# Optimization experiments

Measured on AMD Instinct MI355X. Metric: run time of the kernel, lower is better.

The kernel has to match this reference:

```python
import jax, jax.numpy as jnp
import numpy as np

B, T, C, H, HD = 2, 2048, 2048, 16, 128
RD = HD // 2          # rope_dim = 64 (32 complex pairs)
KVR, QR = 512, 1024   # kv_lora_rank, q_lora_rank


def setup_inputs() -> dict:
    key = jax.random.key(0)
    ks = jax.random.split(key, 10)
    s = 0.02
    x = jax.random.normal(ks[0], (B, T, C), jnp.float32)
    w_dq  = jax.random.normal(ks[1], (C, QR),     jnp.float32) * s
    w_uq  = jax.random.normal(ks[2], (QR, H * HD), jnp.float32) * s
    w_dkv = jax.random.normal(ks[3], (C, KVR),    jnp.float32) * s
    w_uk  = jax.random.normal(ks[4], (KVR, H * HD), jnp.float32) * s
    w_uv  = jax.random.normal(ks[5], (KVR, H * HD), jnp.float32) * s
    w_qr  = jax.random.normal(ks[6], (QR, H * RD), jnp.float32) * s
    w_kr  = jax.random.normal(ks[7], (C, H * RD), jnp.float32) * s
    w_o   = jax.random.normal(ks[8], (H * HD, C), jnp.float32) * s
    # rotary frequencies for the rope_dim part (rope_dim//2 = 32 complex freqs)
    inv_freq = 1.0 / (10000.0 ** (jnp.arange(0, RD, 2, dtype=jnp.float32) / RD))
    ang = jnp.arange(T, dtype=jnp.float32)[:, None] * inv_freq[None, :]  # (T, 32)
    return {"x": x, "w_dq": w_dq, "w_uq": w_uq, "w_dkv": w_dkv, "w_uk": w_uk,
            "w_uv": w_uv, "w_qr": w_qr, "w_kr": w_kr, "w_o": w_o,
            "freqs_cos": jnp.cos(ang), "freqs_sin": jnp.sin(ang)}


def _apply_rope(t, cos, sin):
    # t: (B, T, H, rd); cos/sin: (T, rd//2). Complex rotation on adjacent pairs.
    tr, ti = t[..., 0::2], t[..., 1::2]
    c = cos[None, :, None, :]
    s = sin[None, :, None, :]
    out_r = tr * c - ti * s
    out_i = tr * s + ti * c
    return jnp.stack([out_r, out_i], axis=-1).reshape(t.shape)


def reference(x, w_dq, w_uq, w_dkv, w_uk, w_uv, w_qr, w_kr, w_o, freqs_cos, freqs_sin):
    b, t, _ = x.shape
    # low-rank KV path
    c_kv = x @ w_dkv                                   # (B,T,KVR)
    k_c = (c_kv @ w_uk).reshape(b, t, H, HD)
    v   = (c_kv @ w_uv).reshape(b, t, H, HD)
    # low-rank Q path
    c_q = x @ w_dq                                     # (B,T,QR)
    q_c = (c_q @ w_uq).reshape(b, t, H, HD)
    # decoupled rope parts
    q_r = (c_q @ w_qr).reshape(b, t, H, RD)
    k_r = (x @ w_kr).reshape(b, t, H, RD)
    q_r = _apply_rope(q_r, freqs_cos, freqs_sin)
    k_r = _apply_rope(k_r, freqs_cos, freqs_sin)
    # concat content + rope -> head dim D = HD + RD
    q = jnp.concatenate([q_c, q_r], axis=-1).transpose(0, 2, 1, 3)  # (B,H,T,D)
    k = jnp.concatenate([k_c, k_r], axis=-1).transpose(0, 2, 1, 3)
    v = v.transpose(0, 2, 1, 3)                                     # (B,H,T,HD)
    d = q.shape[-1]
    scores = jnp.einsum('bhqd,bhkd->bhqk', q, k) / jnp.sqrt(jnp.float32(d))
    causal = jnp.tril(jnp.ones((t, t), dtype=bool))
    scores = jnp.where(causal[None, None], scores, jnp.float32(-1e30))
    att = jax.nn.softmax(scores, axis=-1)
    out = jnp.einsum('bhqk,bhkd->bhqd', att, v)        # (B,H,T,HD)
    out = out.transpose(0, 2, 1, 3).reshape(b, t, H * HD)
    return out @ w_o
```

## Files before the change

### kernel.cpp

```cpp
#include <hip/hip_runtime.h>

typedef unsigned short ushort_t;
typedef __attribute__((ext_vector_type(8))) short bs8;
typedef __attribute__((ext_vector_type(4))) float f32x4;
typedef __attribute__((ext_vector_type(4))) unsigned short u16x4;

#define DEV __device__ __forceinline__

DEV unsigned short f2bf(float f){
  unsigned u = __float_as_uint(f);
  u += 0x7fffu + ((u >> 16) & 1u);
  return (unsigned short)(u >> 16);
}
DEV float bf2f(unsigned short h){ return __uint_as_float(((unsigned)h) << 16); }

DEV unsigned cvt_pk_bf16(float lo, float hi){
  unsigned r;
  asm volatile("v_cvt_pk_bf16_f32 %0, %1, %2" : "=v"(r) : "v"(lo), "v"(hi));
  return r;
}

DEV void gl2lds16(const void* g, void* l){
  __builtin_amdgcn_global_load_lds((const __attribute__((address_space(1))) void*)g,
                                   (__attribute__((address_space(3))) void*)l, 16, 0, 0);
}

DEV void st_out(ushort_t* C, size_t i, float v){ C[i] = f2bf(v); }
DEV void st_out(float*    C, size_t i, float v){ C[i] = v; }

__global__ __launch_bounds__(256) void cast_x(const float* __restrict__ in,
                                              ushort_t* __restrict__ outb){
  size_t i = ((size_t)blockIdx.x * 256 + threadIdx.x) * 4;
  float4 v = *(const float4*)(in + i);
  u16x4 o;
  o[0] = f2bf(v.x); o[1] = f2bf(v.y); o[2] = f2bf(v.z); o[3] = f2bf(v.w);
  *(u16x4*)(outb + i) = o;
}

__global__ __launch_bounds__(256) void tcast_all(
    const float* __restrict__ s0, const float* __restrict__ s1,
    const float* __restrict__ s2, const float* __restrict__ s3,
    const float* __restrict__ s4, const float* __restrict__ s5,
    const float* __restrict__ s6, const float* __restrict__ s7,
    ushort_t* __restrict__ d0, ushort_t* __restrict__ d1,
    ushort_t* __restrict__ d2, ushort_t* __restrict__ d3,
    ushort_t* __restrict__ d4, ushort_t* __restrict__ d5,
    ushort_t* __restrict__ d6, ushort_t* __restrict__ d7){
  __shared__ float tile[32][33];
  const int bid = blockIdx.x;
  const float* src; ushort_t* dst; int K, N, loc;
  if      (bid <  2048){ src=s0; dst=d0; K=2048; N=1024; loc=bid; }
  else if (bid <  3072){ src=s1; dst=d1; K=2048; N=512;  loc=bid-2048; }
  else if (bid <  5120){ src=s2; dst=d2; K=2048; N=1024; loc=bid-3072; }
  else if (bid <  7168){ src=s3; dst=d3; K=1024; N=2048; loc=bid-5120; }
  else if (bid <  8192){ src=s4; dst=d4; K=1024; N=1024; loc=bid-7168; }
  else if (bid <  9216){ src=s5; dst=d5; K=512;  N=2048; loc=bid-8192; }
  else if (bid < 10240){ src=s6; dst=d6; K=512;  N=2048; loc=bid-9216; }
  else                 { src=s7; dst=d7; K=2048; N=2048; loc=bid-10240; }
  const int nx = N >> 5;
  const int n0 = (loc % nx) << 5, k0 = (loc / nx) << 5;
  const int tx = threadIdx.x & 31, ty = threadIdx.x >> 5;
  for (int r = ty; r < 32; r += 8)
    tile[r][tx] = src[(size_t)(k0 + r) * N + n0 + tx];
  __syncthreads();
  for (int r = ty; r < 32; r += 8)
    dst[(size_t)(n0 + r) * K + k0 + tx] = f2bf(tile[tx][r]);
}

__global__ __launch_bounds__(256) void transpose_v(const ushort_t* __restrict__ v, int ldv,
                                                   ushort_t* __restrict__ vT){
  __shared__ ushort_t tile[32][33];
  int bh = blockIdx.z; int b = bh >> 4, h = bh & 15;
  int t0 = blockIdx.x * 32, d0 = blockIdx.y * 32;
  int tx = threadIdx.x, ty = threadIdx.y;
  for (int r = ty; r < 32; r += 8)
    tile[r][tx] = v[((size_t)(b * 2048 + t0 + r)) * ldv + h * 128 + d0 + tx];
  __syncthreads();
  for (int r = ty; r < 32; r += 8)
    vT[((size_t)bh * 128 + d0 + r) * 2048 + t0 + tx] = tile[tx][r];
}

DEV void gemm_core(const ushort_t* __restrict__ A, int lda,
                   const ushort_t* __restrict__ BT, int K,
                   int m0, int n0, ushort_t* lds, f32x4 (&acc)[8][4]){
  const int tid = threadIdx.x, lane = tid & 63, wid = tid >> 6;
  const int l15 = lane & 15, lhi = lane >> 4;
  const int wr = wid >> 2, wc = wid & 3;

  const int trow = tid >> 3;
  const int tcsrc = (tid & 7) ^ (trow & 7);
  const ushort_t* gA[2][2];
  const ushort_t* gB[2][2];
#pragma unroll
  for (int h = 0; h < 2; ++h)
#pragma unroll
    for (int i = 0; i < 2; ++i){
      gA[h][i] = A  + (size_t)(m0 + h * 128 + i * 64 + trow) * lda + tcsrc * 8;
      gB[h][i] = BT + (size_t)(n0 + h * 128 + i * 64 + trow) * K   + tcsrc * 8;
    }

  auto STAGE_A = [&](int buf, int h, int kt){
    gl2lds16(gA[h][0] + (size_t)kt * 64, lds + buf * 32768 + h * 8192 + tid * 8);
    gl2lds16(gA[h][1] + (size_t)kt * 64, lds + buf * 32768 + h * 8192 + 4096 + tid * 8);
  };
  auto STAGE_B = [&](int buf, int h, int kt){
    gl2lds16(gB[h][0] + (size_t)kt * 64, lds + buf * 32768 + 16384 + h * 8192 + tid * 8);
    gl2lds16(gB[h][1] + (size_t)kt * 64, lds + buf * 32768 + 16384 + h * 8192 + 4096 + tid * 8);
  };

  const int ck0 = ((lhi) ^ (l15 & 7)) << 3;
  const int ck1 = ((4 + lhi) ^ (l15 & 7)) << 3;

  bs8 aF[4][2], bLo[2][2], bHi[2][2];

  auto RDA = [&](int buf, int mq){
#pragma unroll
    for (int m = 0; m < 4; ++m){
      const ushort_t* r = lds + buf * 32768 + wr * 8192 + ((mq + m) * 16 + l15) * 64;
      aF[m][0] = *(const bs8*)(r + ck0);
      aF[m][1] = *(const bs8*)(r + ck1);
    }
  };
  auto RDB = [&](int buf, int nq, bs8 (&br)[2][2]){
#pragma unroll
    for (int n = 0; n < 2; ++n){
      const ushort_t* r = lds + buf * 32768 + 16384 + (wc >> 1) * 8192 +
                          ((wc & 1) * 64 + (nq + n) * 16 + l15) * 64;
      br[n][0] = *(const bs8*)(r + ck0);
      br[n][1] = *(const bs8*)(r + ck1);
    }
  };
  auto MMA = [&](int mq, int nq, bs8 (&br)[2][2]){
    __builtin_amdgcn_s_setprio(1);
#pragma unroll
    for (int m = 0; m < 4; ++m)
#pragma unroll
      for (int n = 0; n < 2; ++n){
        acc[mq + m][nq + n] = __builtin_amdgcn_mfma_f32_16x16x32_bf16(aF[m][0], br[n][0], acc[mq + m][nq + n], 0, 0, 0);
        acc[mq + m][nq + n] = __builtin_amdgcn_mfma_f32_16x16x32_bf16(aF[m][1], br[n][1], acc[mq + m][nq + n], 0, 0, 0);
      }
    __builtin_amdgcn_s_setprio(0);
  };

#define BAR() __builtin_amdgcn_s_barrier()
#define LGK() asm volatile("s_waitcnt lgkmcnt(0)" ::: "memory")
#define VMC4() asm volatile("s_waitcnt vmcnt(4)" ::: "memory")

  const int nkt = K >> 6;
  const int nIter = K >> 7;

  STAGE_A(0, 0, 0); STAGE_A(0, 1, 0); STAGE_B(0, 0, 0); STAGE_B(0, 1, 0);
  STAGE_B(1, 0, 1); STAGE_B(1, 1, 1);
  VMC4();
  BAR();

  for (int it = 0; it < nIter; ++it){
    const int kt1 = 2 * it + 1;
    int kt2 = 2 * it + 2; if (kt2 > nkt - 1) kt2 = nkt - 1;
    int kt3 = 2 * it + 3; if (kt3 > nkt - 1) kt3 = nkt - 1;
    RDA(0, 0); RDB(0, 0, bLo);
    STAGE_A(1, 0, kt1);
    BAR(); LGK(); MMA(0, 0, bLo); BAR();
    RDB(0, 2, bHi);
    STAGE_A(1, 1, kt1);
    BAR(); LGK(); MMA(0, 2, bHi); BAR();
    RDA(0, 4);
    STAGE_B(0, 0, kt2);
    BAR(); LGK(); MMA(4, 0, bLo); BAR();
    STAGE_B(0, 1, kt2);
    BAR(); LGK(); MMA(4, 2, bHi);
    VMC4(); BAR();
    RDA(1, 0); RDB(1, 0, bLo);
    STAGE_A(0, 0, kt2);
    BAR(); LGK(); MMA(0, 0, bLo); BAR();
    RDB(1, 2, bHi);
    STAGE_A(0, 1, kt2);
    BAR(); LGK(); MMA(0, 2, bHi); BAR();
    RDA(1, 4);
    STAGE_B(1, 0, kt3);
    BAR(); LGK(); MMA(4, 0, bLo); BAR();
    STAGE_B(1, 1, kt3);
    BAR(); LGK(); MMA(4, 2, bHi);
    VMC4(); BAR();
  }
#undef BAR
#undef LGK
#undef VMC4
}

template<int EPI, typename OT>
DEV void gemm_epi(f32x4 (&acc)[8][4], OT* __restrict__ C, int N, int m0, int n0,
                  ushort_t* __restrict__ aux,
                  const float* __restrict__ fcp, const float* __restrict__ fsp){
  const int tid = threadIdx.x, lane = tid & 63, wid = tid >> 6;
  const int l15 = lane & 15, lhi = lane >> 4;
  const int wr = wid >> 2, wc = wid & 3;
  const float SC = (EPI == 2) ? (0.07216878364870323f * 1.4426950408889634f) : 1.0f;
  const int RBASE = (EPI == 1) ? 1536 : 2048;
#pragma unroll
  for (int m = 0; m < 8; ++m){
    const int r = m0 + wr * 128 + m * 16 + lhi * 4;
#pragma unroll
    for (int n = 0; n < 4; ++n){
      const int c = n0 + wc * 64 + n * 16 + l15;
      if (EPI == 0){
#pragma unroll
        for (int j = 0; j < 4; ++j)
          st_out(C, (size_t)(r + j) * N + c, acc[m][n][j]);
      } else if ((EPI == 1 && c < 1536)){
#pragma unroll
        for (int j = 0; j < 4; ++j)
          C[(size_t)(r + j) * 1536 + c] = (OT)f2bf(acc[m][n][j]);
      } else if (EPI == 2 && c < 2048){
        int hh = c >> 7, d = c & 127;
#pragma unroll
        for (int j = 0; j < 4; ++j){
          int rr = r + j, bb = rr >> 11, tt = rr & 2047;
          aux[((size_t)(bb * 16 + hh) * 2048 + tt) * 192 + d] = f2bf(acc[m][n][j] * SC);
        }
      } else if (EPI == 3 && c < 2048){
        int hh = c >> 7, d = c & 127;
#pragma unroll
        for (int j = 0; j < 4; ++j){
          int rr = r + j, bb = rr >> 11, tt = rr & 2047;
          aux[((size_t)(bb * 16 + hh) * 2048 + tt) * 192 + d] = f2bf(acc[m][n][j]);
        }
      } else if (EPI == 3){
#pragma unroll
        for (int j = 0; j < 4; ++j)
          C[(size_t)(r + j) * 2048 + (c - 2048)] = (OT)f2bf(acc[m][n][j]);
      } else {
        int cr = c - RBASE;
        int hh = cr >> 6, dr = cr & 63, ii = dr >> 1;
#pragma unroll
        for (int j = 0; j < 4; ++j){
          int rr = r + j, bb = rr >> 11, tt = rr & 2047;
          float v = acc[m][n][j] * SC;
          float pv = __shfl_xor(v, 1);
          float co = fcp[tt * 32 + ii], si = fsp[tt * 32 + ii];
          float o = (l15 & 1) ? fmaf(pv, si, v * co) : fmaf(-pv, si, v * co);
          aux[((size_t)(bb * 16 + hh) * 2048 + tt) * 192 + 128 + dr] = f2bf(o);
        }
      }
    }
  }
}

template<int EPI, typename OT>
__global__ __launch_bounds__(512, 2) void gemm256(const ushort_t* __restrict__ A, int lda,
                                                  const ushort_t* __restrict__ BT,
                                                  OT* __restrict__ C,
                                                  int M, int N, int K,
                                                  ushort_t* __restrict__ aux,
                                                  const float* __restrict__ fcp,
                                                  const float* __restrict__ fsp){
  __shared__ __align__(16) ushort_t lds[65536];
  const int nbx = M >> 8;
  const int nwg = gridDim.x;
  const int orig = blockIdx.x;
  const int wg = (orig & 7) * (nwg >> 3) + (orig >> 3);
  const int m0 = (wg % nbx) << 8;
  const int n0 = (wg / nbx) << 8;
  f32x4 acc[8][4] = {};
  gemm_core(A, lda, BT, K, m0, n0, lds, acc);
  gemm_epi<EPI, OT>(acc, C, N, m0, n0, aux, fcp, fsp);
}

__global__ __launch_bounds__(512, 2) void gemm23(const ushort_t* __restrict__ A2,
                                                 const ushort_t* __restrict__ BT2,
                                                 const ushort_t* __restrict__ A3,
                                                 const ushort_t* __restrict__ BT3,
                                                 ushort_t* __restrict__ vb,
                                                 ushort_t* __restrict__ Qa,
                                                 ushort_t* __restrict__ Ka,
                                                 const float* __restrict__ fcp,
                                                 const float* __restrict__ fsp){
  __shared__ __align__(16) ushort_t lds[65536];
  const int nwg = gridDim.x;
  const int orig = blockIdx.x;
  const int wg = (orig & 7) * (nwg >> 3) + (orig >> 3);
  f32x4 acc[8][4] = {};
  if (wg < 192){
    const int m0 = (wg % 16) << 8, n0 = (wg / 16) << 8;
    gemm_core(A2, 1536, BT2, 1024, m0, n0, lds, acc);
    gemm_epi<2, ushort_t>(acc, nullptr, 3072, m0, n0, Qa, fcp, fsp);
  } else {
    const int g = wg - 192;
    const int m0 = (g % 16) << 8, n0 = (g / 16) << 8;
    gemm_core(A3, 1536, BT3, 512, m0, n0, lds, acc);
    gemm_epi<3, ushort_t>(acc, vb, 4096, m0, n0, Ka, fcp, fsp);
  }
}

__global__ __launch_bounds__(512, 1) void attn_kernel(const ushort_t* __restrict__ Qa,
                                                      const ushort_t* __restrict__ Ka,
                                                      const ushort_t* __restrict__ VT,
                                                      ushort_t* __restrict__ O){
  __shared__ __align__(16) ushort_t lds[40960 + 34816];
  float* fm = (float*)(lds + 40960);
  const int tid = threadIdx.x, lane = tid & 63, wid = tid >> 6;
  const int sw = wid & 3, par = wid >> 2;
  const int bh = blockIdx.x, p = blockIdx.y;
  const int b = bh >> 4, h = bh & 15;
  const int qb0 = 15 - p, qb1 = p;
  const int nkt0 = 2 * qb0 + 2;
  const int NT = 34;
  const int l15 = lane & 15, lhi = lane >> 4;

  const ushort_t* Kbh = Ka + (size_t)bh * 2048 * 192;
  const ushort_t* Vbh = VT + (size_t)bh * 128 * 2048;

  const ushort_t* ksrc[3];
#pragma unroll
  for (int i = 0; i < 3; ++i){
    int c = i * 512 + tid;
    int row = c / 24, col = c % 24;
    int hk = (row & 3) | (((row >> 3) & 1) << 2);
    ksrc[i] = Kbh + (size_t)row * 192 + (col ^ hk) * 8;
  }
  const ushort_t* vsrc[2];
#pragma unroll
  for (int i = 0; i < 2; ++i){
    int c = i * 512 + tid;
    int d = c >> 3, col = c & 7;
    vsrc[i] = Vbh + (size_t)d * 2048 + (col ^ (d & 7)) * 8;
  }

  auto STAGE = [&](int ft, int buf){
    int kt = (ft < nkt0) ? ft : ft - nkt0;
#pragma unroll
    for (int i = 0; i < 3; ++i)
      gl2lds16(ksrc[i] + (size_t)kt * 12288, lds + buf * 12288 + (i * 512 + tid) * 8);
#pragma unroll
    for (int i = 0; i < 2; ++i)
      gl2lds16(vsrc[i] + kt * 64, lds + 24576 + buf * 8192 + (i * 512 + tid) * 8);
  };

  bs8 qf[2][6];
  auto LOADQ = [&](int qb){
#pragma unroll
    for (int qg = 0; qg < 2; ++qg){
      const size_t qrow = ((size_t)bh * 2048 + qb * 128 + sw * 32 + qg * 16 + l15) * 192;
#pragma unroll
      for (int kc = 0; kc < 6; ++kc)
        qf[qg][kc] = *(const bs8*)(Qa + qrow + kc * 32 + lhi * 8);
    }
  };

  f32x4 acc[2][8] = {};
  float mrow[2] = {-1e30f, -1e30f};
  float lrow[2] = {0.f, 0.f};

  auto MERGE_EPI = [&](int qb){
    if (par == 1){
#pragma unroll
      for (int qg = 0; qg < 2; ++qg)
#pragma unroll
        for (int f = 0; f < 8; ++f)
          *(f32x4*)(fm + sw * 4096 + (qg * 8 + f) * 256 + lane * 4) = acc[qg][f];
      f32x4 ml;
      ml[0] = mrow[0]; ml[1] = lrow[0]; ml[2] = mrow[1]; ml[3] = lrow[1];
      *(f32x4*)(fm + 16384 + sw * 256 + lane * 4) = ml;
    }
    __syncthreads();
    if (par == 0){
      f32x4 ml = *(const f32x4*)(fm + 16384 + sw * 256 + lane * 4);
#pragma unroll
      for (int qg = 0; qg < 2; ++qg){
        float m1 = ml[2 * qg], l1 = ml[2 * qg + 1];
        float mm = fmaxf(mrow[qg], m1);
        float f0 = exp2f(mrow[qg] - mm), f1v = exp2f(m1 - mm);
        float rl = 1.0f / (lrow[qg] * f0 + l1 * f1v);
        int t = qb * 128 + sw * 32 + qg * 16 + l15;
#pragma unroll
        for (int f = 0; f < 8; ++f){
          f32x4 a1 = *(const f32x4*)(fm + sw * 4096 + (qg * 8 + f) * 256 + lane * 4);
          u16x4 o;
#pragma unroll
          for (int j = 0; j < 4; ++j)
            o[j] = f2bf((acc[qg][f][j] * f0 + a1[j] * f1v) * rl);
          *(u16x4*)(O + ((size_t)b * 2048 + t) * 2048 + h * 128 + f * 16 + lhi * 4) = o;
        }
      }
    }
  };

  const int hkr = (l15 & 3) | (((l15 >> 2) & 1) << 2);

#define BARR() __builtin_amdgcn_s_barrier()
#define LGK0() asm volatile("s_waitcnt lgkmcnt(0)" ::: "memory")
#define VMC(n) asm volatile("s_waitcnt vmcnt(" #n ")" ::: "memory")

  LOADQ(qb0);
  STAGE(0, 0);
  STAGE(1, 1);
  VMC(5);
  BARR();

  for (int ft = 0; ft < NT; ++ft){
    if (ft == nkt0){
      MERGE_EPI(qb0);
#pragma unroll
      for (int qg = 0; qg < 2; ++qg)
#pragma unroll
        for (int f = 0; f < 8; ++f) acc[qg][f] = (f32x4){0.f, 0.f, 0.f, 0.f};
      mrow[0] = mrow[1] = -1e30f; lrow[0] = lrow[1] = 0.f;
      LOADQ(qb1);
    }
    const int seg = (ft >= nkt0) ? 1 : 0;
    const int kt = seg ? ft - nkt0 : ft;
    const int qb = seg ? qb1 : qb0;
    const int qm0 = qb << 7;
    const int mylast = 2 * qb + (sw >> 1);
    const int cur = ft & 1;
    const ushort_t* Kb = lds + cur * 12288;
    const ushort_t* Vb = lds + 24576 + cur * 8192;

    if (((kt & 1) == par) && kt <= mylast){
      f32x4 s[2][4] = {};
      __builtin_amdgcn_s_setprio(1);
#pragma unroll
      for (int kc = 0; kc < 6; ++kc){
        bs8 kf4[4];
#pragma unroll
        for (int m = 0; m < 4; ++m){
          int row = ((m >> 1) << 5) + ((l15 >> 2) << 3) + ((m & 1) << 2) + (l15 & 3);
          kf4[m] = *(const bs8*)(Kb + row * 192 + (((kc * 4 + lhi) ^ hkr) << 3));
        }
#pragma unroll
        for (int qg = 0; qg < 2; ++qg)
#pragma unroll
          for (int m = 0; m < 4; ++m)
            s[qg][m] = __builtin_amdgcn_mfma_f32_16x16x32_bf16(kf4[m], qf[qg][kc], s[qg][m], 0, 0, 0);
      }
      __builtin_amdgcn_s_setprio(0);

      const bool noMask = (kt * 64 + 63) <= (qm0 + sw * 32);
      bs8 pb[2][2];
#pragma unroll
      for (int qg = 0; qg < 2; ++qg){
        const int qi = qm0 + sw * 32 + qg * 16 + l15;
        float rmax = -3e38f;
#pragma unroll
        for (int m = 0; m < 4; ++m)
#pragma unroll
          for (int j = 0; j < 4; ++j){
            float sv = s[qg][m][j];
            if (!noMask){
              int ki = kt * 64 + ((m >> 1) << 5) + (lhi << 3) + ((m & 1) << 2) + j;
              if (ki > qi) sv = -3e38f;
            }
            s[qg][m][j] = sv;
            rmax = fmaxf(rmax, sv);
          }
        rmax = fmaxf(rmax, __shfl_xor(rmax, 16));
        rmax = fmaxf(rmax, __shfl_xor(rmax, 32));
        if (!__all(rmax <= mrow[qg] + 8.f)){
          float mnew = fmaxf(mrow[qg], rmax);
          float osc = exp2f(mrow[qg] - mnew);
          lrow[qg] *= osc;
#pragma unroll
          for (int f = 0; f < 8; ++f) acc[qg][f] *= osc;
          mrow[qg] = mnew;
        }
        float rsum = 0.f;
#pragma unroll
        for (int m = 0; m < 4; ++m)
#pragma unroll
          for (int j = 0; j < 4; ++j){
            float pv = exp2f(s[qg][m][j] - mrow[qg]);
            s[qg][m][j] = pv;
            rsum += pv;
          }
        rsum += __shfl_xor(rsum, 16);
        rsum += __shfl_xor(rsum, 32);
        lrow[qg] += rsum;

#pragma unroll
        for (int kc2 = 0; kc2 < 2; ++kc2){
          union { bs8 v; unsigned u[4]; } pu;
#pragma unroll
          for (int half = 0; half < 2; ++half){
            const f32x4& sv = s[qg][2 * kc2 + half];
            pu.u[2 * half]     = cvt_pk_bf16(sv[0], sv[1]);
            pu.u[2 * half + 1] = cvt_pk_bf16(sv[2], sv[3]);
          }
          pb[qg][kc2] = pu.v;
        }
      }

      __builtin_amdgcn_s_setprio(1);
#pragma unroll
      for (int kc2 = 0; kc2 < 2; ++kc2)
#pragma unroll
        for (int f = 0; f < 8; ++f){
          bs8 vf = *(const bs8*)(Vb + (f * 16 + l15) * 64 + (((kc2 * 4 + lhi) ^ (l15 & 7)) << 3));
#pragma unroll
          for (int qg = 0; qg < 2; ++qg)
            acc[qg][f] = __builtin_amdgcn_mfma_f32_16x16x32_bf16(vf, pb[qg][kc2], acc[qg][f], 0, 0, 0);
        }
      __builtin_amdgcn_s_setprio(0);
    }

    LGK0();
    BARR();
    if (ft + 2 < NT){
      STAGE(ft + 2, cur);
      VMC(5);
    } else {
      VMC(0);
    }
    BARR();
  }
#undef BARR
#undef LGK0
#undef VMC

  MERGE_EPI(qb1);
}

extern "C" void kernel_launch(void* const* d_in, const int* in_sizes, int n_in,
                              void* d_out, int out_size, void* d_ws, size_t ws_size,
                              hipStream_t stream){
  constexpr int Bc = 2, Tc = 2048, Cc = 2048, Hc = 16, HDc = 128, RDc = 64, KVRc = 512, QRc = 1024;
  constexpr int Mx = Bc * Tc;
  const float* x     = (const float*)d_in[0];
  const float* w_dq  = (const float*)d_in[1];
  const float* w_uq  = (const float*)d_in[2];
  const float* w_dkv = (const float*)d_in[3];
  const float* w_uk  = (const float*)d_in[4];
  const float* w_uv  = (const float*)d_in[5];
  const float* w_qr  = (const float*)d_in[6];
  const float* w_kr  = (const float*)d_in[7];
  const float* w_o   = (const float*)d_in[8];
  const float* fc    = (const float*)d_in[9];
  const float* fs    = (const float*)d_in[10];
  float* out = (float*)d_out;

  char* ws = (char*)d_ws;
  size_t off = 0;
  auto alloc = [&](size_t elems) -> ushort_t* {
    ushort_t* p = (ushort_t*)(ws + off);
    off += ((elems * 2) + 255) & ~(size_t)255;
    return p;
  };
  ushort_t* xb    = alloc((size_t)Mx * Cc);
  ushort_t* wdqT  = alloc((size_t)QRc * Cc);
  ushort_t* wdkvT = alloc((size_t)KVRc * Cc);
  ushort_t* wkrT  = alloc((size_t)(Hc * RDc) * Cc);
  ushort_t* wuqT  = alloc((size_t)(Hc * HDc) * QRc);
  ushort_t* wqrT  = alloc((size_t)(Hc * RDc) * QRc);
  ushort_t* wukT  = alloc((size_t)(Hc * HDc) * KVRc);
  ushort_t* wuvT  = alloc((size_t)(Hc * HDc) * KVRc);
  ushort_t* woT   = alloc((size_t)Cc * (Hc * HDc));
  ushort_t* comb1 = alloc((size_t)Mx * 1536);
  ushort_t* vb    = alloc((size_t)Mx * 2048);
  ushort_t* Qa    = alloc((size_t)Bc * Hc * Tc * 192);
  ushort_t* Ka    = alloc((size_t)Bc * Hc * Tc * 192);
  ushort_t* vT    = alloc((size_t)Bc * Hc * HDc * Tc);
  ushort_t* O     = xb;

  cast_x<<<dim3(((size_t)Mx * Cc) / 1024), 256, 0, stream>>>(x, xb);

  tcast_all<<<dim3(14336), 256, 0, stream>>>(w_dq, w_dkv, w_kr, w_uq, w_qr, w_uk, w_uv, w_o,
                                             wdqT, wdkvT, wkrT, wuqT, wqrT, wukT, wuvT, woT);

  gemm256<1, ushort_t><<<dim3((Mx / 256) * (2560 / 256)), 512, 0, stream>>>(
      xb, Cc, wdqT, comb1, Mx, 2560, Cc, Ka, fc, fs);
  gemm23<<<dim3(448), 512, 0, stream>>>(comb1, wuqT, comb1 + QRc, wukT, vb, Qa, Ka, fc, fs);

  transpose_v<<<dim3(Tc / 32, HDc / 32, Bc * Hc), dim3(32, 8), 0, stream>>>(vb, 2048, vT);

  attn_kernel<<<dim3(Bc * Hc, 8), 512, 0, stream>>>(Qa, Ka, vT, O);

  gemm256<0, float><<<dim3((Mx / 256) * (Cc / 256)), 512, 0, stream>>>(
      O, Hc * HDc, woT, out, Mx, Cc, Hc * HDc, nullptr, nullptr, nullptr);
}
```

Before: 333.9 us.

## Split attention by query rows per wave and add 256x128-tile output GEMM

The attention kernel stops splitting K tiles between two wave groups, which then had to merge their partial softmax states through LDS. Now each of the 8 waves owns 16 query rows and walks every K tile, so the merge pass, its extra LDS and its block barrier go away. The cost is a longer serial loop per wave, and more waves sit idle near the causal diagonal. The output projection moves to a new 256x128-tile GEMM with a finer interleaved LDS pipeline, launching 256 workgroups instead of 128 to fill more CUs.

After: 306.5 us. 8.2% less time.

```diff
diff --git a/kernel.cpp b/kernel.cpp
--- a/kernel.cpp
+++ b/kernel.cpp
@@ -292,14 +292,142 @@
   }
 }
 
+__global__ __launch_bounds__(512, 1) void gemm4_128(const ushort_t* __restrict__ A, int lda,
+                                                    const ushort_t* __restrict__ BT,
+                                                    float* __restrict__ C,
+                                                    int M, int N, int K){
+  __shared__ __align__(16) ushort_t lds[49152];
+  const int tid = threadIdx.x, lane = tid & 63, wid = tid >> 6;
+  const int l15 = lane & 15, lhi = lane >> 4;
+  const int wr = wid >> 1, wc = wid & 1;
+
+  const int nbx = M >> 8;
+  const int nwg = gridDim.x;
+  const int orig = blockIdx.x;
+  const int wg = (orig & 7) * (nwg >> 3) + (orig >> 3);
+  const int m0 = (wg % nbx) << 8;
+  const int n0 = (wg / nbx) << 7;
+
+  const int trow = tid >> 3;
+  const int tcsrc = (tid & 7) ^ (trow & 7);
+  const ushort_t* gA[2][2];
+  const ushort_t* gB[2];
+#pragma unroll
+  for (int h = 0; h < 2; ++h)
+#pragma unroll
+    for (int i = 0; i < 2; ++i)
+      gA[h][i] = A + (size_t)(m0 + h * 128 + i * 64 + trow) * lda + tcsrc * 8;
+#pragma unroll
+  for (int i = 0; i < 2; ++i)
+    gB[i] = BT + (size_t)(n0 + i * 64 + trow) * K + tcsrc * 8;
+
+  auto STAGE_A = [&](int buf, int h, int kt){
+    gl2lds16(gA[h][0] + (size_t)kt * 64, lds + buf * 24576 + h * 8192 + tid * 8);
+    gl2lds16(gA[h][1] + (size_t)kt * 64, lds + buf * 24576 + h * 8192 + 4096 + tid * 8);
+  };
+  auto STAGE_B = [&](int buf, int kt){
+    gl2lds16(gB[0] + (size_t)kt * 64, lds + buf * 24576 + 16384 + tid * 8);
+    gl2lds16(gB[1] + (size_t)kt * 64, lds + buf * 24576 + 16384 + 4096 + tid * 8);
+  };
+
+  const int ck0 = ((lhi) ^ (l15 & 7)) << 3;
+  const int ck1 = ((4 + lhi) ^ (l15 & 7)) << 3;
+
+  f32x4 acc[4][4] = {};
+  bs8 aF[2][2], bLo[2][2], bHi[2][2];
+
+  auto RDA = [&](int buf, int mq){
+#pragma unroll
+    for (int m = 0; m < 2; ++m){
+      const int rowin = (wr & 1) * 64 + (mq + m) * 16 + l15;
+      const ushort_t* r = lds + buf * 24576 + (wr >> 1) * 8192 + rowin * 64;
+      aF[m][0] = *(const bs8*)(r + ck0);
+      aF[m][1] = *(const bs8*)(r + ck1);
+    }
+  };
+  auto RDB = [&](int buf, int nq, bs8 (&br)[2][2]){
+#pragma unroll
+    for (int n = 0; n < 2; ++n){
+      const int row = wc * 64 + (nq + n) * 16 + l15;
+      const ushort_t* r = lds + buf * 24576 + 16384 + row * 64;
+      br[n][0] = *(const bs8*)(r + ck0);
+      br[n][1] = *(const bs8*)(r + ck1);
+    }
+  };
+  auto MMA = [&](int mq, int nq, bs8 (&br)[2][2]){
+    __builtin_amdgcn_s_setprio(1);
+#pragma unroll
+    for (int m = 0; m < 2; ++m)
+#pragma unroll
+      for (int n = 0; n < 2; ++n){
+        acc[mq + m][nq + n] = __builtin_amdgcn_mfma_f32_16x16x32_bf16(aF[m][0], br[n][0], acc[mq + m][nq + n], 0, 0, 0);
+        acc[mq + m][nq + n] = __builtin_amdgcn_mfma_f32_16x16x32_bf16(aF[m][1], br[n][1], acc[mq + m][nq + n], 0, 0, 0);
+      }
+    __builtin_amdgcn_s_setprio(0);
+  };
+
+#define BAR() __builtin_amdgcn_s_barrier()
+#define LGK() asm volatile("s_waitcnt lgkmcnt(0)" ::: "memory")
+#define VMC2() asm volatile("s_waitcnt vmcnt(2)" ::: "memory")
+
+  const int nkt = K >> 6;
+  const int nIter = K >> 7;
+
+  STAGE_A(0, 0, 0); STAGE_A(0, 1, 0); STAGE_B(0, 0);
+  STAGE_B(1, 1);
+  VMC2();
+  BAR();
+
+  for (int it = 0; it < nIter; ++it){
+    const int kt1 = 2 * it + 1;
+    int kt2 = 2 * it + 2; if (kt2 > nkt - 1) kt2 = nkt - 1;
+    int kt3 = 2 * it + 3; if (kt3 > nkt - 1) kt3 = nkt - 1;
+    RDA(0, 0); RDB(0, 0, bLo);
+    STAGE_A(1, 0, kt1);
+    BAR(); LGK(); MMA(0, 0, bLo); BAR();
+    RDB(0, 2, bHi);
+    STAGE_A(1, 1, kt1);
+    BAR(); LGK(); MMA(0, 2, bHi); BAR();
+    RDA(0, 2);
+    STAGE_B(0, kt2);
+    BAR(); LGK(); MMA(2, 0, bLo); BAR();
+    BAR(); LGK(); MMA(2, 2, bHi);
+    VMC2(); BAR();
+    RDA(1, 0); RDB(1, 0, bLo);
+    STAGE_A(0, 0, kt2);
+    BAR(); LGK(); MMA(0, 0, bLo); BAR();
+    RDB(1, 2, bHi);
+    STAGE_A(0, 1, kt2);
+    BAR(); LGK(); MMA(0, 2, bHi); BAR();
+    RDA(1, 2);
+    STAGE_B(1, kt3);
+    BAR(); LGK(); MMA(2, 0, bLo); BAR();
+    BAR(); LGK(); MMA(2, 2, bHi);
+    VMC2(); BAR();
+  }
+#undef BAR
+#undef LGK
+#undef VMC2
+
+#pragma unroll
+  for (int m = 0; m < 4; ++m){
+    const int r = m0 + wr * 64 + m * 16 + lhi * 4;
+#pragma unroll
+    for (int n = 0; n < 4; ++n){
+      const int c = n0 + wc * 64 + n * 16 + l15;
+#pragma unroll
+      for (int j = 0; j < 4; ++j)
+        C[(size_t)(r + j) * N + c] = acc[m][n][j];
+    }
+  }
+}
+
 __global__ __launch_bounds__(512, 1) void attn_kernel(const ushort_t* __restrict__ Qa,
                                                       const ushort_t* __restrict__ Ka,
                                                       const ushort_t* __restrict__ VT,
                                                       ushort_t* __restrict__ O){
-  __shared__ __align__(16) ushort_t lds[40960 + 34816];
-  float* fm = (float*)(lds + 40960);
+  __shared__ __align__(16) ushort_t lds[40960];
   const int tid = threadIdx.x, lane = tid & 63, wid = tid >> 6;
-  const int sw = wid & 3, par = wid >> 2;
   const int bh = blockIdx.x, p = blockIdx.y;
   const int b = bh >> 4, h = bh & 15;
   const int qb0 = 15 - p, qb1 = p;
@@ -336,52 +464,26 @@
       gl2lds16(vsrc[i] + kt * 64, lds + 24576 + buf * 8192 + (i * 512 + tid) * 8);
   };
 
-  bs8 qf[2][6];
+  bs8 qf[6];
   auto LOADQ = [&](int qb){
-#pragma unroll
-    for (int qg = 0; qg < 2; ++qg){
-      const size_t qrow = ((size_t)bh * 2048 + qb * 128 + sw * 32 + qg * 16 + l15) * 192;
-#pragma unroll
-      for (int kc = 0; kc < 6; ++kc)
-        qf[qg][kc] = *(const bs8*)(Qa + qrow + kc * 32 + lhi * 8);
-    }
-  };
-
-  f32x4 acc[2][8] = {};
-  float mrow[2] = {-1e30f, -1e30f};
-  float lrow[2] = {0.f, 0.f};
-
-  auto MERGE_EPI = [&](int qb){
-    if (par == 1){
-#pragma unroll
-      for (int qg = 0; qg < 2; ++qg)
-#pragma unroll
-        for (int f = 0; f < 8; ++f)
-          *(f32x4*)(fm + sw * 4096 + (qg * 8 + f) * 256 + lane * 4) = acc[qg][f];
-      f32x4 ml;
-      ml[0] = mrow[0]; ml[1] = lrow[0]; ml[2] = mrow[1]; ml[3] = lrow[1];
-      *(f32x4*)(fm + 16384 + sw * 256 + lane * 4) = ml;
-    }
-    __syncthreads();
-    if (par == 0){
-      f32x4 ml = *(const f32x4*)(fm + 16384 + sw * 256 + lane * 4);
-#pragma unroll
-      for (int qg = 0; qg < 2; ++qg){
-        float m1 = ml[2 * qg], l1 = ml[2 * qg + 1];
-        float mm = fmaxf(mrow[qg], m1);
-        float f0 = exp2f(mrow[qg] - mm), f1v = exp2f(m1 - mm);
-        float rl = 1.0f / (lrow[qg] * f0 + l1 * f1v);
-        int t = qb * 128 + sw * 32 + qg * 16 + l15;
-#pragma unroll
-        for (int f = 0; f < 8; ++f){
-          f32x4 a1 = *(const f32x4*)(fm + sw * 4096 + (qg * 8 + f) * 256 + lane * 4);
-          u16x4 o;
-#pragma unroll
-          for (int j = 0; j < 4; ++j)
-            o[j] = f2bf((acc[qg][f][j] * f0 + a1[j] * f1v) * rl);
-          *(u16x4*)(O + ((size_t)b * 2048 + t) * 2048 + h * 128 + f * 16 + lhi * 4) = o;
-        }
-      }
+    const size_t qrow = ((size_t)bh * 2048 + qb * 128 + wid * 16 + l15) * 192;
+#pragma unroll
+    for (int kc = 0; kc < 6; ++kc)
+      qf[kc] = *(const bs8*)(Qa + qrow + kc * 32 + lhi * 8);
+  };
+
+  f32x4 acc[8] = {};
+  float mrow = -1e30f, lrow = 0.f;
+
+  auto EPI = [&](int qb){
+    float rl = 1.0f / lrow;
+    int t = qb * 128 + wid * 16 + l15;
+#pragma unroll
+    for (int f = 0; f < 8; ++f){
+      u16x4 o;
+#pragma unroll
+      for (int j = 0; j < 4; ++j) o[j] = f2bf(acc[f][j] * rl);
+      *(u16x4*)(O + ((size_t)b * 2048 + t) * 2048 + h * 128 + f * 16 + lhi * 4) = o;
     }
   };
 
@@ -399,25 +501,23 @@
 
   for (int ft = 0; ft < NT; ++ft){
     if (ft == nkt0){
-      MERGE_EPI(qb0);
-#pragma unroll
-      for (int qg = 0; qg < 2; ++qg)
-#pragma unroll
-        for (int f = 0; f < 8; ++f) acc[qg][f] = (f32x4){0.f, 0.f, 0.f, 0.f};
-      mrow[0] = mrow[1] = -1e30f; lrow[0] = lrow[1] = 0.f;
+      EPI(qb0);
+#pragma unroll
+      for (int f = 0; f < 8; ++f) acc[f] = (f32x4){0.f, 0.f, 0.f, 0.f};
+      mrow = -1e30f; lrow = 0.f;
       LOADQ(qb1);
     }
     const int seg = (ft >= nkt0) ? 1 : 0;
     const int kt = seg ? ft - nkt0 : ft;
     const int qb = seg ? qb1 : qb0;
     const int qm0 = qb << 7;
-    const int mylast = 2 * qb + (sw >> 1);
+    const int mylast = 2 * qb + (wid >> 2);
     const int cur = ft & 1;
     const ushort_t* Kb = lds + cur * 12288;
     const ushort_t* Vb = lds + 24576 + cur * 8192;
 
-    if (((kt & 1) == par) && kt <= mylast){
-      f32x4 s[2][4] = {};
+    if (kt <= mylast){
+      f32x4 s[4] = {};
       __builtin_amdgcn_s_setprio(1);
 #pragma unroll
       for (int kc = 0; kc < 6; ++kc){
@@ -428,65 +528,60 @@
           kf4[m] = *(const bs8*)(Kb + row * 192 + (((kc * 4 + lhi) ^ hkr) << 3));
         }
 #pragma unroll
-        for (int qg = 0; qg < 2; ++qg)
-#pragma unroll
-          for (int m = 0; m < 4; ++m)
-            s[qg][m] = __builtin_amdgcn_mfma_f32_16x16x32_bf16(kf4[m], qf[qg][kc], s[qg][m], 0, 0, 0);
+        for (int m = 0; m < 4; ++m)
+          s[m] = __builtin_amdgcn_mfma_f32_16x16x32_bf16(kf4[m], qf[kc], s[m], 0, 0, 0);
       }
       __builtin_amdgcn_s_setprio(0);
 
-      const bool noMask = (kt * 64 + 63) <= (qm0 + sw * 32);
-      bs8 pb[2][2];
-#pragma unroll
-      for (int qg = 0; qg < 2; ++qg){
-        const int qi = qm0 + sw * 32 + qg * 16 + l15;
-        float rmax = -3e38f;
-#pragma unroll
-        for (int m = 0; m < 4; ++m)
-#pragma unroll
-          for (int j = 0; j < 4; ++j){
-            float sv = s[qg][m][j];
-            if (!noMask){
-              int ki = kt * 64 + ((m >> 1) << 5) + (lhi << 3) + ((m & 1) << 2) + j;
-              if (ki > qi) sv = -3e38f;
-            }
-            s[qg][m][j] = sv;
-            rmax = fmaxf(rmax, sv);
+      const bool noMask = (kt * 64 + 63) <= (qm0 + wid * 16);
+      const int qi = qm0 + wid * 16 + l15;
+      float rmax = -3e38f;
+#pragma unroll
+      for (int m = 0; m < 4; ++m)
+#pragma unroll
+        for (int j = 0; j < 4; ++j){
+          float sv = s[m][j];
+          if (!noMask){
+            int ki = kt * 64 + ((m >> 1) << 5) + (lhi << 3) + ((m & 1) << 2) + j;
+            if (ki > qi) sv = -3e38f;
           }
-        rmax = fmaxf(rmax, __shfl_xor(rmax, 16));
-        rmax = fmaxf(rmax, __shfl_xor(rmax, 32));
-        if (!__all(rmax <= mrow[qg] + 8.f)){
-          float mnew = fmaxf(mrow[qg], rmax);
-          float osc = exp2f(mrow[qg] - mnew);
-          lrow[qg] *= osc;
-#pragma unroll
-          for (int f = 0; f < 8; ++f) acc[qg][f] *= osc;
-          mrow[qg] = mnew;
-        }
-        float rsum = 0.f;
-#pragma unroll
-        for (int m = 0; m < 4; ++m)
-#pragma unroll
-          for (int j = 0; j < 4; ++j){
-            float pv = exp2f(s[qg][m][j] - mrow[qg]);
-            s[qg][m][j] = pv;
-            rsum += pv;
-          }
-        rsum += __shfl_xor(rsum, 16);
-        rsum += __shfl_xor(rsum, 32);
-        lrow[qg] += rsum;
-
-#pragma unroll
-        for (int kc2 = 0; kc2 < 2; ++kc2){
-          union { bs8 v; unsigned u[4]; } pu;
-#pragma unroll
-          for (int half = 0; half < 2; ++half){
-            const f32x4& sv = s[qg][2 * kc2 + half];
-            pu.u[2 * half]     = cvt_pk_bf16(sv[0], sv[1]);
-            pu.u[2 * half + 1] = cvt_pk_bf16(sv[2], sv[3]);
-          }
-          pb[qg][kc2] = pu.v;
-        }
+          s[m][j] = sv;
+          rmax = fmaxf(rmax, sv);
+        }
+      rmax = fmaxf(rmax, __shfl_xor(rmax, 16));
+      rmax = fmaxf(rmax, __shfl_xor(rmax, 32));
+      if (!__all(rmax <= mrow + 8.f)){
+        float mnew = fmaxf(mrow, rmax);
+        float osc = exp2f(mrow - mnew);
+        lrow *= osc;
+#pragma unroll
+        for (int f = 0; f < 8; ++f) acc[f] *= osc;
+        mrow = mnew;
+      }
+      float rsum = 0.f;
+#pragma unroll
+      for (int m = 0; m < 4; ++m)
+#pragma unroll
+        for (int j = 0; j < 4; ++j){
+          float pv = exp2f(s[m][j] - mrow);
+          s[m][j] = pv;
+          rsum += pv;
+        }
+      rsum += __shfl_xor(rsum, 16);
+      rsum += __shfl_xor(rsum, 32);
+      lrow += rsum;
+
+      bs8 pb[2];
+#pragma unroll
+      for (int kc2 = 0; kc2 < 2; ++kc2){
+        union { bs8 v; unsigned u[4]; } pu;
+#pragma unroll
+        for (int half = 0; half < 2; ++half){
+          const f32x4& sv = s[2 * kc2 + half];
+          pu.u[2 * half]     = cvt_pk_bf16(sv[0], sv[1]);
+          pu.u[2 * half + 1] = cvt_pk_bf16(sv[2], sv[3]);
+        }
+        pb[kc2] = pu.v;
       }
 
       __builtin_amdgcn_s_setprio(1);
@@ -495,9 +590,7 @@
 #pragma unroll
         for (int f = 0; f < 8; ++f){
           bs8 vf = *(const bs8*)(Vb + (f * 16 + l15) * 64 + (((kc2 * 4 + lhi) ^ (l15 & 7)) << 3));
-#pragma unroll
-          for (int qg = 0; qg < 2; ++qg)
-            acc[qg][f] = __builtin_amdgcn_mfma_f32_16x16x32_bf16(vf, pb[qg][kc2], acc[qg][f], 0, 0, 0);
+          acc[f] = __builtin_amdgcn_mfma_f32_16x16x32_bf16(vf, pb[kc2], acc[f], 0, 0, 0);
         }
       __builtin_amdgcn_s_setprio(0);
     }
@@ -516,7 +609,7 @@
 #undef LGK0
 #undef VMC
 
-  MERGE_EPI(qb1);
+  EPI(qb1);
 }
 
 extern "C" void kernel_launch(void* const* d_in, const int* in_sizes, int n_in,
@@ -573,6 +666,5 @@
 
   attn_kernel<<<dim3(Bc * Hc, 8), 512, 0, stream>>>(Qa, Ka, vT, O);
 
-  gemm256<0, float><<<dim3((Mx / 256) * (Cc / 256)), 512, 0, stream>>>(
-      O, Hc * HDc, woT, out, Mx, Cc, Hc * HDc, nullptr, nullptr, nullptr);
-}
+  gemm4_128<<<dim3(256), 512, 0, stream>>>(O, Hc * HDc, woT, out, Mx, Cc, Hc * HDc);
+}
```
